# Kernel tuning notes

Hardware: AMD Instinct MI355X
Metric: run time of the kernel (lower is better)

Reference implementation:

```python
import jax, jax.numpy as jnp
import numpy as np

D_IN = 1024
D_OUT = 1024
NUM_HEADS = 16
DIM_HEAD = D_OUT // NUM_HEADS


def setup_inputs() -> dict:
    key = jax.random.key(0)
    ks = jax.random.split(key, 6)
    s = 0.02
    x = jax.random.normal(ks[0], (2, 2048, D_IN), dtype=jnp.float32)
    Wk = jax.random.normal(ks[1], (D_IN, D_OUT), dtype=jnp.float32) * s
    Wq = jax.random.normal(ks[2], (D_IN, D_OUT), dtype=jnp.float32) * s
    Wv = jax.random.normal(ks[3], (D_IN, D_OUT), dtype=jnp.float32) * s
    Wo = jax.random.normal(ks[4], (D_OUT, D_OUT), dtype=jnp.float32) * s
    bo = jax.random.normal(ks[5], (D_OUT,), dtype=jnp.float32) * s
    return {"x": x, "Wk": Wk, "Wq": Wq, "Wv": Wv, "Wo": Wo, "bo": bo}


def reference(x, Wk, Wq, Wv, Wo, bo):
    B, S, _ = x.shape
    # projections -> [B, H, S, Dh]
    def split_heads(t):
        return t.reshape(B, S, NUM_HEADS, DIM_HEAD).transpose(0, 2, 1, 3)
    q = split_heads(x @ Wq)
    k = split_heads(x @ Wk)
    v = split_heads(x @ Wv)
    # NOTE: source uses non-in-place masked_fill whose result is discarded,
    # so NO causal mask is actually applied (faithful reproduction).
    scores = jnp.einsum("bhqd,bhkd->bhqk", q, k) / jnp.sqrt(jnp.float32(DIM_HEAD))
    wgts = jax.nn.softmax(scores, axis=-1)  # dropout = identity (eval mode)
    ctx = jnp.einsum("bhqk,bhkd->bhqd", wgts, v)
    ctx = ctx.transpose(0, 2, 1, 3).reshape(B, S, D_OUT)
    return ctx @ Wo + bo
```

## Files before the change

### kernel.cpp

```cpp
#include <hip/hip_runtime.h>
#include <stdint.h>

typedef short bf16x8 __attribute__((ext_vector_type(8)));
typedef float f32x4  __attribute__((ext_vector_type(4)));
typedef unsigned int u32x4 __attribute__((ext_vector_type(4)));
typedef unsigned int u32x2 __attribute__((ext_vector_type(2)));

__device__ __forceinline__ unsigned short f2bf(float f) {
  unsigned int u = __builtin_bit_cast(unsigned int, f) + 0x8000u;
  return (unsigned short)(u >> 16);
}
__device__ __forceinline__ unsigned int pack2bf(float a, float b) {
  unsigned int ua = __builtin_bit_cast(unsigned int, a) + 0x8000u;
  unsigned int ub = __builtin_bit_cast(unsigned int, b) + 0x8000u;
  return __builtin_amdgcn_perm(ub, ua, 0x07060302);
}

__device__ __forceinline__ void gl2lds16(const void* g, void* l) {
  __builtin_amdgcn_global_load_lds(
      (const __attribute__((address_space(1))) void*)g,
      (__attribute__((address_space(3))) void*)l, 16, 0, 0);
}

template <int N> __device__ __forceinline__ void wait_vmcnt() {
  asm volatile("s_waitcnt vmcnt(%0)" ::"n"(N) : "memory");
}

__global__ __launch_bounds__(256) void cast_x_k(const float* __restrict__ x,
                                                unsigned short* __restrict__ xb) {
  int i = blockIdx.x * 256 + threadIdx.x;
  float4 v = ((const float4*)x)[i];
  u32x2 o;
  o.x = pack2bf(v.x, v.y);
  o.y = pack2bf(v.z, v.w);
  ((u32x2*)xb)[i] = o;
}

__global__ __launch_bounds__(256) void castT_k(
    const float* __restrict__ Wq, const float* __restrict__ Wk,
    const float* __restrict__ Wv, const float* __restrict__ Wo,
    unsigned short* __restrict__ Tq, unsigned short* __restrict__ Tk,
    unsigned short* __restrict__ Tv, unsigned short* __restrict__ To) {
  __shared__ float tile[32][33];
  const int z = blockIdx.z;
  const float* W = (z == 0) ? Wq : (z == 1) ? Wk : (z == 2) ? Wv : Wo;
  unsigned short* T = (z == 0) ? Tq : (z == 1) ? Tk : (z == 2) ? Tv : To;
  const int tx = threadIdx.x, ty = threadIdx.y;
  const int n0 = blockIdx.x * 32, k0 = blockIdx.y * 32;
#pragma unroll
  for (int j = 0; j < 32; j += 8)
    tile[ty + j][tx] = W[(size_t)(k0 + ty + j) * 1024 + n0 + tx];
  __syncthreads();
#pragma unroll
  for (int j = 0; j < 32; j += 8)
    T[(size_t)(n0 + ty + j) * 1024 + k0 + tx] = f2bf(tile[tx][ty + j]);
}

template <int MODE, int TN>
__global__ __launch_bounds__(256) void gemm_bt_k(const unsigned short* __restrict__ A,
                                                 const unsigned short* __restrict__ B,
                                                 void* __restrict__ C,
                                                 const float* __restrict__ bias,
                                                 int K) {
  __shared__ alignas(16) short lA[3][512 * 8];
  __shared__ alignas(16) short lB[3][128 * TN * 8];
  constexpr int PT = 2 + TN / 2;
  const int tid = threadIdx.x;
  const int wid = tid >> 6, lane = tid & 63;
  const int l15 = lane & 15, quad = lane >> 4;
  const int waveM = wid >> 1, waveN = wid & 1;
  const int bm = blockIdx.y * 128, bn = blockIdx.x * (32 * TN);

  f32x4 acc[4][TN];
#pragma unroll
  for (int i = 0; i < 4; ++i)
#pragma unroll
    for (int j = 0; j < TN; ++j) acc[i][j] = (f32x4){0.f, 0.f, 0.f, 0.f};

  auto stage = [&](int kk, short* la, short* lb) {
#pragma unroll
    for (int j = 0; j < 2; ++j) {
      int c = tid + 256 * j;
      int row = ((c >> 6) << 4) | (c & 15);
      int ch = (c >> 4) & 3;
      gl2lds16(A + (size_t)(bm + row) * K + kk + ch * 8, &la[(c & ~63) * 8]);
    }
#pragma unroll
    for (int j = 0; j < TN / 2; ++j) {
      int c = tid + 256 * j;
      int row = ((c >> 6) << 4) | (c & 15);
      int ch = (c >> 4) & 3;
      gl2lds16(B + (size_t)(bn + row) * K + kk + ch * 8, &lb[(c & ~63) * 8]);
    }
  };

  auto compute = [&](const short* la, const short* lb) {
    bf16x8 af[4], bfr[TN];
#pragma unroll
    for (int i = 0; i < 4; ++i)
      af[i] = *(const bf16x8*)&la[(((waveM * 4 + i) * 64) + lane) * 8];
#pragma unroll
    for (int j = 0; j < TN; ++j)
      bfr[j] = *(const bf16x8*)&lb[(((waveN * TN + j) * 64) + lane) * 8];
#pragma unroll
    for (int i = 0; i < 4; ++i)
#pragma unroll
      for (int j = 0; j < TN; ++j)
        acc[i][j] = __builtin_amdgcn_mfma_f32_16x16x32_bf16(af[i], bfr[j], acc[i][j], 0, 0, 0);
  };

  const int NT = K >> 5;
  short *pa0 = lA[0], *pa1 = lA[1], *pa2 = lA[2];
  short *pb0 = lB[0], *pb1 = lB[1], *pb2 = lB[2];
  stage(0, pa0, pb0);
  stage(32, pa1, pb1);
#pragma unroll 1
  for (int t = 0; t < NT - 1; ++t) {
    wait_vmcnt<PT>();
    __builtin_amdgcn_sched_barrier(0);
    __builtin_amdgcn_s_barrier();
    __builtin_amdgcn_sched_barrier(0);
    if (t + 2 < NT) stage((t + 2) * 32, pa2, pb2);
    compute(pa0, pb0);
    short* ta = pa0; pa0 = pa1; pa1 = pa2; pa2 = ta;
    short* tb = pb0; pb0 = pb1; pb1 = pb2; pb2 = tb;
  }
  wait_vmcnt<0>();
  __builtin_amdgcn_sched_barrier(0);
  __builtin_amdgcn_s_barrier();
  __builtin_amdgcn_sched_barrier(0);
  compute(pa0, pb0);

#pragma unroll
  for (int i = 0; i < 4; ++i)
#pragma unroll
    for (int j = 0; j < TN; ++j) {
      int row = bm + waveM * 64 + i * 16 + quad * 4;
      int col = bn + (waveN * TN + j) * 16 + l15;
      if (MODE == 0) {
        unsigned short* Cq = (unsigned short*)C;
        int w = col >> 10, n1 = col & 1023;
        int h = n1 >> 6, d = n1 & 63;
        int b = row >> 11, s = row & 2047;
        int bhh = (b << 4) + h;
        if (w == 2) {
          int g = (i << 2) + quad;
          int ks2 = g >> 3, rem = g & 7;
          int pos = ((ks2 << 2) + (rem & 3)) * 8 + (rem >> 2) * 4;
          u32x2 pk;
          pk.x = pack2bf(acc[i][j][0], acc[i][j][1]);
          pk.y = pack2bf(acc[i][j][2], acc[i][j][3]);
          *(u32x2*)&Cq[(size_t)2 * 4194304 + ((size_t)bhh * 64 + d) * 2048 +
                       (s & ~63) + pos] = pk;
        } else {
          float sc = (w == 0) ? 0.18033688011112042f : 1.0f;
#pragma unroll
          for (int r = 0; r < 4; ++r)
            Cq[(size_t)w * 4194304 + ((size_t)bhh * 2048 + s + r) * 64 + d] =
                f2bf(acc[i][j][r] * sc);
        }
      } else {
#pragma unroll
        for (int r = 0; r < 4; ++r)
          ((float*)C)[(size_t)(row + r) * 1024 + col] = acc[i][j][r] + bias[col];
      }
    }
}

__global__ __launch_bounds__(256) void flash_k(const unsigned short* __restrict__ Qh,
                                               const unsigned short* __restrict__ Kh,
                                               const unsigned short* __restrict__ Vt,
                                               unsigned short* __restrict__ ctxb) {
  constexpr int SL = 2048;
  __shared__ alignas(16) short kt[3][512 * 8];
  __shared__ alignas(16) short vt[3][512 * 8];

  const int tid = threadIdx.x;
  const int wid = tid >> 6, lane = tid & 63;
  const int l15 = lane & 15, quad = lane >> 4;
  const int bid = blockIdx.x;
  const int jj = bid >> 3;
  const int bh = ((bid & 7) << 2) | (jj >> 4);
  const int q0 = (jj & 15) * 128 + wid * 32;

  const unsigned short* Qb = Qh + (size_t)bh * SL * 64;
  const unsigned short* Kb = Kh + (size_t)bh * SL * 64;
  const unsigned short* Vb = Vt + (size_t)bh * 64 * SL;

  bf16x8 qf[2][2];
#pragma unroll
  for (int s = 0; s < 2; ++s)
#pragma unroll
    for (int ks = 0; ks < 2; ++ks)
      qf[s][ks] = *(const bf16x8*)(Qb + (size_t)(q0 + s * 16 + l15) * 64 + ks * 32 + quad * 8);

  f32x4 o[2][4];
  f32x4 rs4[2] = {(f32x4){0.f, 0.f, 0.f, 0.f}, (f32x4){0.f, 0.f, 0.f, 0.f}};
  const f32x4 z4 = (f32x4){0.f, 0.f, 0.f, 0.f};
#pragma unroll
  for (int s = 0; s < 2; ++s)
#pragma unroll
    for (int t = 0; t < 4; ++t) o[s][t] = z4;

  auto stage = [&](int kb, short* ktb, short* vtb) {
#pragma unroll
    for (int j2 = 0; j2 < 2; ++j2) {
      int cc = tid + 256 * j2;
      int row = cc >> 3;
      int ko = (cc & 7) ^ (row & 7);
      gl2lds16(Kb + (size_t)(kb + row) * 64 + ko * 8, &ktb[(cc & ~63) * 8]);
      gl2lds16(Vb + (size_t)row * SL + kb + ko * 8, &vtb[(cc & ~63) * 8]);
    }
  };

  auto compute = [&](const short* ktb, const short* vtb) {
    f32x4 sv[2][4];
#pragma unroll
    for (int t = 0; t < 4; ++t) {
      int key = t * 16 + l15;
      bf16x8 kf0 = *(bf16x8*)&ktb[(key * 8 + (quad ^ (key & 7))) * 8];
      bf16x8 kf1 = *(bf16x8*)&ktb[(key * 8 + ((4 + quad) ^ (key & 7))) * 8];
#pragma unroll
      for (int s = 0; s < 2; ++s) {
        sv[s][t] = __builtin_amdgcn_mfma_f32_16x16x32_bf16(kf0, qf[s][0], z4, 0, 0, 0);
        sv[s][t] = __builtin_amdgcn_mfma_f32_16x16x32_bf16(kf1, qf[s][1], sv[s][t], 0, 0, 0);
      }
    }
    u32x4 pf[2][2];
#pragma unroll
    for (int s = 0; s < 2; ++s)
#pragma unroll
      for (int t = 0; t < 4; ++t) {
        f32x4 p;
#pragma unroll
        for (int r = 0; r < 4; ++r) p[r] = __builtin_amdgcn_exp2f(sv[s][t][r]);
        rs4[s] += p;
        pf[s][t >> 1][(t & 1) * 2 + 0] = pack2bf(p[0], p[1]);
        pf[s][t >> 1][(t & 1) * 2 + 1] = pack2bf(p[2], p[3]);
      }
#pragma unroll
    for (int t = 0; t < 4; ++t) {
      int d = t * 16 + l15;
#pragma unroll
      for (int ks = 0; ks < 2; ++ks) {
        bf16x8 vf = *(bf16x8*)&vtb[(d * 8 + ((ks * 4 + quad) ^ (d & 7))) * 8];
#pragma unroll
        for (int s = 0; s < 2; ++s)
          o[s][t] = __builtin_amdgcn_mfma_f32_16x16x32_bf16(
              vf, __builtin_bit_cast(bf16x8, pf[s][ks]), o[s][t], 0, 0, 0);
      }
    }
  };

  short *k0 = kt[0], *k1 = kt[1], *k2 = kt[2];
  short *v0 = vt[0], *v1 = vt[1], *v2 = vt[2];
  stage(0, k0, v0);
  stage(64, k1, v1);
#pragma unroll 1
  for (int t = 0; t < 31; ++t) {
    wait_vmcnt<4>();
    __builtin_amdgcn_sched_barrier(0);
    __builtin_amdgcn_s_barrier();
    __builtin_amdgcn_sched_barrier(0);
    if (t + 2 < 32) stage((t + 2) * 64, k2, v2);
    compute(k0, v0);
    short* tk = k0; k0 = k1; k1 = k2; k2 = tk;
    short* tv = v0; v0 = v1; v1 = v2; v2 = tv;
  }
  wait_vmcnt<0>();
  __builtin_amdgcn_sched_barrier(0);
  __builtin_amdgcn_s_barrier();
  __builtin_amdgcn_sched_barrier(0);
  compute(k0, v0);

  const int bb = bh >> 4, h = bh & 15;
#pragma unroll
  for (int s = 0; s < 2; ++s) {
    float v = (rs4[s][0] + rs4[s][1]) + (rs4[s][2] + rs4[s][3]);
    v += __shfl_xor(v, 16);
    v += __shfl_xor(v, 32);
    float inv = 1.0f / v;
    int tok = q0 + s * 16 + l15;
    size_t base = ((size_t)(bb * 2048 + tok)) * 1024 + h * 64;
#pragma unroll
    for (int t = 0; t < 4; ++t) {
      u32x2 pk;
      pk.x = pack2bf(o[s][t][0] * inv, o[s][t][1] * inv);
      pk.y = pack2bf(o[s][t][2] * inv, o[s][t][3] * inv);
      *(u32x2*)&ctxb[base + t * 16 + quad * 4] = pk;
    }
  }
}

extern "C" void kernel_launch(void* const* d_in, const int* in_sizes, int n_in,
                              void* d_out, int out_size, void* d_ws, size_t ws_size,
                              hipStream_t stream) {
  const float* x  = (const float*)d_in[0];
  const float* Wk = (const float*)d_in[1];
  const float* Wq = (const float*)d_in[2];
  const float* Wv = (const float*)d_in[3];
  const float* Wo = (const float*)d_in[4];
  const float* bo = (const float*)d_in[5];
  float* out = (float*)d_out;

  char* ws = (char*)d_ws;
  const size_t MB = 1u << 20;
  unsigned short* xb   = (unsigned short*)(ws);
  unsigned short* WqT  = (unsigned short*)(ws + 8  * MB);
  unsigned short* WkT  = (unsigned short*)(ws + 10 * MB);
  unsigned short* WvT  = (unsigned short*)(ws + 12 * MB);
  unsigned short* WoT  = (unsigned short*)(ws + 14 * MB);
  unsigned short* Qh   = (unsigned short*)(ws + 16 * MB);
  unsigned short* ctxb = xb;

  cast_x_k<<<4096, 256, 0, stream>>>(x, xb);
  castT_k<<<dim3(32, 32, 4), dim3(32, 8), 0, stream>>>(Wq, Wk, Wv, Wo, WqT, WkT, WvT, WoT);
  gemm_bt_k<0, 4><<<dim3(24, 32), 256, 0, stream>>>(xb, WqT, Qh, nullptr, 1024);
  flash_k<<<512, 256, 0, stream>>>(Qh, Qh + 4194304, Qh + 2 * 4194304, ctxb);
  gemm_bt_k<1, 2><<<dim3(16, 32), 256, 0, stream>>>(ctxb, WoT, out, bo, 1024);
}
```

Before: 211.7 us.

## Deepen LDS prefetch to four buffers and widen QKV GEMM tile

Both the GEMM and flash-attention kernels move from a three-buffer to a four-buffer LDS ring. Each iteration now issues its prefetch before the vmcnt wait and barrier, so two tiles stay in flight during compute. The QKV projection GEMM grows its N-tile from 4 to 6 fragments per wave, cutting the grid to 16x32. A minimum of two blocks per CU is requested through launch bounds. The risks are higher LDS and register pressure, possible spills under the tighter launch bounds, and fewer blocks for the QKV GEMM.

```diff
diff --git a/kernel.cpp b/kernel.cpp
--- a/kernel.cpp
+++ b/kernel.cpp
@@ -57,13 +57,13 @@
 }
 
 template <int MODE, int TN>
-__global__ __launch_bounds__(256) void gemm_bt_k(const unsigned short* __restrict__ A,
-                                                 const unsigned short* __restrict__ B,
-                                                 void* __restrict__ C,
-                                                 const float* __restrict__ bias,
-                                                 int K) {
-  __shared__ alignas(16) short lA[3][512 * 8];
-  __shared__ alignas(16) short lB[3][128 * TN * 8];
+__global__ __launch_bounds__(256, 2) void gemm_bt_k(const unsigned short* __restrict__ A,
+                                                    const unsigned short* __restrict__ B,
+                                                    void* __restrict__ C,
+                                                    const float* __restrict__ bias,
+                                                    int K) {
+  __shared__ alignas(16) short lA[4][512 * 8];
+  __shared__ alignas(16) short lB[4][128 * TN * 8];
   constexpr int PT = 2 + TN / 2;
   const int tid = threadIdx.x;
   const int wid = tid >> 6, lane = tid & 63;
@@ -110,21 +110,28 @@
   };
 
   const int NT = K >> 5;
-  short *pa0 = lA[0], *pa1 = lA[1], *pa2 = lA[2];
-  short *pb0 = lB[0], *pb1 = lB[1], *pb2 = lB[2];
+  short *pa0 = lA[0], *pa1 = lA[1], *pa2 = lA[2], *pa3 = lA[3];
+  short *pb0 = lB[0], *pb1 = lB[1], *pb2 = lB[2], *pb3 = lB[3];
   stage(0, pa0, pb0);
   stage(32, pa1, pb1);
 #pragma unroll 1
-  for (int t = 0; t < NT - 1; ++t) {
-    wait_vmcnt<PT>();
+  for (int t = 0; t < NT - 2; ++t) {
+    stage((t + 2) * 32, pa2, pb2);
+    wait_vmcnt<2 * PT>();
     __builtin_amdgcn_sched_barrier(0);
     __builtin_amdgcn_s_barrier();
     __builtin_amdgcn_sched_barrier(0);
-    if (t + 2 < NT) stage((t + 2) * 32, pa2, pb2);
     compute(pa0, pb0);
-    short* ta = pa0; pa0 = pa1; pa1 = pa2; pa2 = ta;
-    short* tb = pb0; pb0 = pb1; pb1 = pb2; pb2 = tb;
+    short* ta = pa0; pa0 = pa1; pa1 = pa2; pa2 = pa3; pa3 = ta;
+    short* tb = pb0; pb0 = pb1; pb1 = pb2; pb2 = pb3; pb3 = tb;
   }
+  wait_vmcnt<PT>();
+  __builtin_amdgcn_sched_barrier(0);
+  __builtin_amdgcn_s_barrier();
+  __builtin_amdgcn_sched_barrier(0);
+  compute(pa0, pb0);
+  { short* ta = pa0; pa0 = pa1; pa1 = pa2; pa2 = pa3; pa3 = ta;
+    short* tb = pb0; pb0 = pb1; pb1 = pb2; pb2 = pb3; pb3 = tb; }
   wait_vmcnt<0>();
   __builtin_amdgcn_sched_barrier(0);
   __builtin_amdgcn_s_barrier();
@@ -167,13 +174,13 @@
     }
 }
 
-__global__ __launch_bounds__(256) void flash_k(const unsigned short* __restrict__ Qh,
-                                               const unsigned short* __restrict__ Kh,
-                                               const unsigned short* __restrict__ Vt,
-                                               unsigned short* __restrict__ ctxb) {
+__global__ __launch_bounds__(256, 2) void flash_k(const unsigned short* __restrict__ Qh,
+                                                  const unsigned short* __restrict__ Kh,
+                                                  const unsigned short* __restrict__ Vt,
+                                                  unsigned short* __restrict__ ctxb) {
   constexpr int SL = 2048;
-  __shared__ alignas(16) short kt[3][512 * 8];
-  __shared__ alignas(16) short vt[3][512 * 8];
+  __shared__ alignas(16) short kt[4][512 * 8];
+  __shared__ alignas(16) short vt[4][512 * 8];
 
   const int tid = threadIdx.x;
   const int wid = tid >> 6, lane = tid & 63;
@@ -252,21 +259,28 @@
     }
   };
 
-  short *k0 = kt[0], *k1 = kt[1], *k2 = kt[2];
-  short *v0 = vt[0], *v1 = vt[1], *v2 = vt[2];
+  short *k0 = kt[0], *k1 = kt[1], *k2 = kt[2], *k3 = kt[3];
+  short *v0 = vt[0], *v1 = vt[1], *v2 = vt[2], *v3 = vt[3];
   stage(0, k0, v0);
   stage(64, k1, v1);
 #pragma unroll 1
-  for (int t = 0; t < 31; ++t) {
-    wait_vmcnt<4>();
+  for (int t = 0; t < 30; ++t) {
+    stage((t + 2) * 64, k2, v2);
+    wait_vmcnt<8>();
     __builtin_amdgcn_sched_barrier(0);
     __builtin_amdgcn_s_barrier();
     __builtin_amdgcn_sched_barrier(0);
-    if (t + 2 < 32) stage((t + 2) * 64, k2, v2);
     compute(k0, v0);
-    short* tk = k0; k0 = k1; k1 = k2; k2 = tk;
-    short* tv = v0; v0 = v1; v1 = v2; v2 = tv;
+    short* tk = k0; k0 = k1; k1 = k2; k2 = k3; k3 = tk;
+    short* tv = v0; v0 = v1; v1 = v2; v2 = v3; v3 = tv;
   }
+  wait_vmcnt<4>();
+  __builtin_amdgcn_sched_barrier(0);
+  __builtin_amdgcn_s_barrier();
+  __builtin_amdgcn_sched_barrier(0);
+  compute(k0, v0);
+  { short* tk = k0; k0 = k1; k1 = k2; k2 = k3; k3 = tk;
+    short* tv = v0; v0 = v1; v1 = v2; v2 = v3; v3 = tv; }
   wait_vmcnt<0>();
   __builtin_amdgcn_sched_barrier(0);
   __builtin_amdgcn_s_barrier();
@@ -315,7 +329,7 @@
 
   cast_x_k<<<4096, 256, 0, stream>>>(x, xb);
   castT_k<<<dim3(32, 32, 4), dim3(32, 8), 0, stream>>>(Wq, Wk, Wv, Wo, WqT, WkT, WvT, WoT);
-  gemm_bt_k<0, 4><<<dim3(24, 32), 256, 0, stream>>>(xb, WqT, Qh, nullptr, 1024);
+  gemm_bt_k<0, 6><<<dim3(16, 32), 256, 0, stream>>>(xb, WqT, Qh, nullptr, 1024);
   flash_k<<<512, 256, 0, stream>>>(Qh, Qh + 4194304, Qh + 2 * 4194304, ctxb);
   gemm_bt_k<1, 2><<<dim3(16, 32), 256, 0, stream>>>(ctxb, WoT, out, bo, 1024);
 }
```

Measured after the change: 198.1 us. -6.4%, faster.
